# Kernel tuning notes

Hardware: AMD Instinct MI355X
Metric: run time of the kernel (lower is better)

## Reference

```python
import jax, jax.numpy as jnp
import numpy as np

WIDTHS = [2, 3, 5, 8, 13, 21, 34, 55, 89, 26]  # ragged one-hot feature widths, sum = 256
NSEG = len(WIDTHS)
B, IN = 8192, 256
LAYOUT = [1024, 1024, 1024, 256]
EPS = 1e-5  # BatchNorm1d default eps
TAU = 1.0


def setup_inputs() -> dict:
    key = jax.random.key(0)
    ks = iter(jax.random.split(key, 64))
    inp = {"x": jax.random.normal(next(ks), (B, IN), jnp.float32)}
    prev = IN
    for i, fc in enumerate(LAYOUT):
        inp[f"W{i}"] = jax.random.normal(next(ks), (fc, prev), jnp.float32) / np.float32(np.sqrt(prev))
        inp[f"b{i}"] = 0.01 * jax.random.normal(next(ks), (fc,), jnp.float32)
        if i + 1 < len(LAYOUT):  # Residual blocks carry BatchNorm params (eval mode)
            inp[f"g{i}"] = 1.0 + 0.1 * jax.random.normal(next(ks), (fc,), jnp.float32)
            inp[f"be{i}"] = 0.1 * jax.random.normal(next(ks), (fc,), jnp.float32)
            inp[f"rm{i}"] = 0.1 * jax.random.normal(next(ks), (fc,), jnp.float32)
            inp[f"rv{i}"] = 0.75 + 0.5 * jax.random.uniform(next(ks), (fc,), dtype=jnp.float32)
        prev += fc
    inp["seg_ids"] = jnp.asarray(np.repeat(np.arange(NSEG), WIDTHS), jnp.int32)  # [256]
    return inp


def _residual(x, W, b, g, be, rm, rv):
    # Linear -> eval-mode BatchNorm1d -> ReLU -> concat([out, input])
    h = x @ W.T + b
    h = (h - rm) * (g * jax.lax.rsqrt(rv + EPS)) + be
    return jnp.concatenate([jax.nn.relu(h), x], axis=1)


def _segment_softmax(x, seg_ids):
    # Fused segmented softmax over ragged feature groups (replaces per-feature Python loop)
    xt = x.T / TAU                                            # [F, B]
    m = jax.ops.segment_max(xt, seg_ids, num_segments=NSEG)   # [NSEG, B]
    e = jnp.exp(xt - m[seg_ids])
    s = jax.ops.segment_sum(e, seg_ids, num_segments=NSEG)
    return (e / s[seg_ids]).T                                 # [B, F]


def reference(x, W0, b0, g0, be0, rm0, rv0, W1, b1, g1, be1, rm1, rv1,
              W2, b2, g2, be2, rm2, rv2, W3, b3, seg_ids):
    h = _residual(x, W0, b0, g0, be0, rm0, rv0)   # [B, 1280]
    h = _residual(h, W1, b1, g1, be1, rm1, rv1)   # [B, 2304]
    h = _residual(h, W2, b2, g2, be2, rm2, rv2)   # [B, 3328]
    h = h @ W3.T + b3                              # [B, 256]
    return _segment_softmax(h, seg_ids)
```

## Files before the change

### kernel.cpp

```cpp
#include <hip/hip_runtime.h>
#include <hip/hip_fp16.h>


#define LDH 3328
#define NROWS 8192

typedef _Float16 f16x8 __attribute__((ext_vector_type(8)));
typedef _Float16 f16x4 __attribute__((ext_vector_type(4)));
typedef float f32x4 __attribute__((ext_vector_type(4)));

__constant__ int c_bnd[11] = {0, 2, 5, 10, 18, 31, 52, 86, 141, 230, 256};

__device__ __forceinline__ void async_cp16(const _Float16* g, _Float16* l) {
  __builtin_amdgcn_global_load_lds(
      (__attribute__((address_space(1))) void*)g,
      (__attribute__((address_space(3))) void*)l, 16, 0, 0);
}

__device__ __forceinline__ _Float16 f2h(float f) { return (_Float16)f; }

__global__ void prep_kernel(const float* __restrict__ s0,
                            const float* __restrict__ s1,
                            const float* __restrict__ s2,
                            const float* __restrict__ s3,
                            const float* __restrict__ x,
                            const float* __restrict__ b3,
                            _Float16* __restrict__ d0,
                            _Float16* __restrict__ d1,
                            _Float16* __restrict__ d2,
                            _Float16* __restrict__ d3,
                            _Float16* __restrict__ H, float* __restrict__ out,
                            int n0, int n1, int n2, int n3, int n4, int n5) {
  int i = blockIdx.x * blockDim.x + threadIdx.x;
  if (i >= n5) return;
  if (i >= n4) {
    const int j = i - n4;
    const int c = (j & 63) * 4;
    *(float4*)&out[(size_t)j * 4] = *(const float4*)&b3[c];
    return;
  }
  if (i >= n3) {
    const int j = i - n3;
    const int row = j >> 6;
    const int c = (j & 63) * 4;
    const float4 v = *(const float4*)&x[(size_t)j * 4];
    f16x4 h = {f2h(v.x), f2h(v.y), f2h(v.z), f2h(v.w)};
    *(f16x4*)&H[(size_t)row * LDH + 3072 + c] = h;
    return;
  }
  const float* s;
  _Float16* d;
  if (i < n0) {
    s = s0; d = d0;
  } else if (i < n1) {
    s = s1 - (size_t)n0 * 4; d = d1 - (size_t)n0 * 4;
  } else if (i < n2) {
    s = s2 - (size_t)n1 * 4; d = d2 - (size_t)n1 * 4;
  } else {
    s = s3 - (size_t)n2 * 4; d = d3 - (size_t)n2 * 4;
  }
  const float4 v = *(const float4*)&s[(size_t)i * 4];
  f16x4 h = {f2h(v.x), f2h(v.y), f2h(v.z), f2h(v.w)};
  *(f16x4*)&d[(size_t)i * 4] = h;
}

__launch_bounds__(256, 2) __global__
void gemm_bn_kernel(const _Float16* __restrict__ A, int K,
                    const _Float16* __restrict__ W,
                    const float* __restrict__ bias,
                    const float* __restrict__ g, const float* __restrict__ be,
                    const float* __restrict__ rm,
                    const float* __restrict__ rv, _Float16* __restrict__ outH,
                    int outOff) {
  __shared__ _Float16 Alds[128 * 128];
  __shared__ _Float16 Blds[128 * 128];

  const int tid = threadIdx.x;
  const int lane = tid & 63;
  const int wave = tid >> 6;
  const int wr = wave >> 1;
  const int wc = wave & 1;
  const int row0 = blockIdx.x * 128;
  const int col0 = blockIdx.y * 128;
  const int lr4 = lane >> 4;
  const int sl = lane & 15;
  const int fr = lane & 15;
  const int q = lane >> 4;

  f32x4 acc[4][4] = {};

  for (int k0 = 0; k0 < K; k0 += 128) {
    __syncthreads();
#pragma unroll
    for (int it = 0; it < 8; ++it) {
      const int j = it * 4 + wave;
      const int r = j * 4 + lr4;
      const int gc = sl ^ (r & 7);
      async_cp16(A + (size_t)(row0 + r) * LDH + k0 + gc * 8, &Alds[j * 512]);
      async_cp16(W + (size_t)(col0 + r) * K + k0 + gc * 8, &Blds[j * 512]);
    }
    __syncthreads();

#pragma unroll
    for (int kq = 0; kq < 4; ++kq) {
      f16x8 av[4], bv[4];
#pragma unroll
      for (int t = 0; t < 4; ++t) {
        const int ra = wr * 64 + t * 16 + fr;
        av[t] =
            *(const f16x8*)&Alds[ra * 128 + (((kq * 4 + q) ^ (ra & 7)) * 8)];
        const int rb = wc * 64 + t * 16 + fr;
        bv[t] =
            *(const f16x8*)&Blds[rb * 128 + (((kq * 4 + q) ^ (rb & 7)) * 8)];
      }
#pragma unroll
      for (int tm = 0; tm < 4; ++tm)
#pragma unroll
        for (int tn = 0; tn < 4; ++tn)
          acc[tm][tn] = __builtin_amdgcn_mfma_f32_16x16x32_f16(
              av[tm], bv[tn], acc[tm][tn], 0, 0, 0);
    }
  }

#pragma unroll
  for (int tn = 0; tn < 4; ++tn) {
    const int n = col0 + wc * 64 + tn * 16 + fr;
    const float alpha = g[n] * rsqrtf(rv[n] + 1e-5f);
    const float beta = (bias[n] - rm[n]) * alpha + be[n];
#pragma unroll
    for (int tm = 0; tm < 4; ++tm) {
      const int rbase = row0 + wr * 64 + tm * 16 + q * 4;
#pragma unroll
      for (int r = 0; r < 4; ++r) {
        float v = acc[tm][tn][r] * alpha + beta;
        v = fmaxf(v, 0.0f);
        outH[(size_t)(rbase + r) * LDH + outOff + n] = f2h(v);
      }
    }
  }
}

__launch_bounds__(256, 4) __global__
void gemm_out_kernel(const _Float16* __restrict__ A,
                     const _Float16* __restrict__ W,
                     float* __restrict__ out) {
  __shared__ _Float16 Alds[128 * 64];
  __shared__ _Float16 Blds[128 * 64];

  const int tid = threadIdx.x;
  const int lane = tid & 63;
  const int wave = tid >> 6;
  const int wr = wave >> 1;
  const int wc = wave & 1;
  const int row0 = blockIdx.x * 128;
  const int cb = blockIdx.y & 1;
  const int ks = blockIdx.y >> 1;
  const int col0 = cb * 128;
  const int k0b = ks * 832;
  const int k0e = k0b + 832;
  const int lr = lane >> 3;
  const int ls = lane & 7;
  const int lc = ls ^ lr;
  const int fr = lane & 15;
  const int q = lane >> 4;
  const int K = 3328;

  f32x4 acc[4][4] = {};

  for (int k0 = k0b; k0 < k0e; k0 += 64) {
    __syncthreads();
#pragma unroll
    for (int it = 0; it < 4; ++it) {
      const int rl = it * 32 + wave * 8;
      async_cp16(A + (size_t)(row0 + rl + lr) * LDH + k0 + lc * 8,
                 &Alds[rl * 64]);
      async_cp16(W + (size_t)(col0 + rl + lr) * K + k0 + lc * 8,
                 &Blds[rl * 64]);
    }
    __syncthreads();

#pragma unroll
    for (int kq = 0; kq < 2; ++kq) {
      f16x8 av[4], bv[4];
#pragma unroll
      for (int t = 0; t < 4; ++t) {
        const int ra = wr * 64 + t * 16 + fr;
        av[t] = *(const f16x8*)&Alds[ra * 64 + (((q + 4 * kq) ^ (ra & 7)) * 8)];
        const int rb = wc * 64 + t * 16 + fr;
        bv[t] = *(const f16x8*)&Blds[rb * 64 + (((q + 4 * kq) ^ (rb & 7)) * 8)];
      }
#pragma unroll
      for (int tm = 0; tm < 4; ++tm)
#pragma unroll
        for (int tn = 0; tn < 4; ++tn)
          acc[tm][tn] = __builtin_amdgcn_mfma_f32_16x16x32_f16(
              av[tm], bv[tn], acc[tm][tn], 0, 0, 0);
    }
  }

#pragma unroll
  for (int tn = 0; tn < 4; ++tn) {
    const int n = col0 + wc * 64 + tn * 16 + fr;
#pragma unroll
    for (int tm = 0; tm < 4; ++tm) {
      const int rbase = row0 + wr * 64 + tm * 16 + q * 4;
#pragma unroll
      for (int r = 0; r < 4; ++r)
        atomicAdd(&out[(size_t)(rbase + r) * 256 + n], acc[tm][tn][r]);
    }
  }
}

__global__ void segsoftmax_kernel(float* __restrict__ out,
                                  const int* __restrict__ segids) {
  __shared__ float vals[4][256];
  __shared__ float red[4][10];
  const int w = threadIdx.x >> 6;
  const int l = threadIdx.x & 63;
  const int row = blockIdx.x * 4 + w;
  float4 v = *(float4*)&out[(size_t)row * 256 + l * 4];
  *(float4*)&vals[w][l * 4] = v;
  __syncthreads();
  if (l < 10) {
    float m = -1e30f;
    for (int j = c_bnd[l]; j < c_bnd[l + 1]; ++j) m = fmaxf(m, vals[w][j]);
    red[w][l] = m;
  }
  __syncthreads();
  const int4 s4 = *(const int4*)&segids[l * 4];
  float4 e;
  e.x = expf(v.x - red[w][s4.x]);
  e.y = expf(v.y - red[w][s4.y]);
  e.z = expf(v.z - red[w][s4.z]);
  e.w = expf(v.w - red[w][s4.w]);
  *(float4*)&vals[w][l * 4] = e;
  __syncthreads();
  if (l < 10) {
    float s = 0.0f;
    for (int j = c_bnd[l]; j < c_bnd[l + 1]; ++j) s += vals[w][j];
    red[w][l] = s;
  }
  __syncthreads();
  float4 o;
  o.x = e.x / red[w][s4.x];
  o.y = e.y / red[w][s4.y];
  o.z = e.z / red[w][s4.z];
  o.w = e.w / red[w][s4.w];
  *(float4*)&out[(size_t)row * 256 + l * 4] = o;
}

extern "C" void kernel_launch(void* const* d_in, const int* in_sizes, int n_in,
                              void* d_out, int out_size, void* d_ws,
                              size_t ws_size, hipStream_t stream) {
  const float* x = (const float*)d_in[0];
  const float* W0 = (const float*)d_in[1];
  const float* b0 = (const float*)d_in[2];
  const float* g0 = (const float*)d_in[3];
  const float* be0 = (const float*)d_in[4];
  const float* rm0 = (const float*)d_in[5];
  const float* rv0 = (const float*)d_in[6];
  const float* W1 = (const float*)d_in[7];
  const float* b1 = (const float*)d_in[8];
  const float* g1 = (const float*)d_in[9];
  const float* be1 = (const float*)d_in[10];
  const float* rm1 = (const float*)d_in[11];
  const float* rv1 = (const float*)d_in[12];
  const float* W2 = (const float*)d_in[13];
  const float* b2 = (const float*)d_in[14];
  const float* g2 = (const float*)d_in[15];
  const float* be2 = (const float*)d_in[16];
  const float* rm2 = (const float*)d_in[17];
  const float* rv2 = (const float*)d_in[18];
  const float* W3 = (const float*)d_in[19];
  const float* b3 = (const float*)d_in[20];
  const int* seg = (const int*)d_in[21];
  float* out = (float*)d_out;

  _Float16* H = (_Float16*)d_ws;
  size_t off = (size_t)NROWS * LDH;
  _Float16* Wh0 = H + off; off += 1024 * 256;
  _Float16* Wh1 = H + off; off += 1024 * 1280;
  _Float16* Wh2 = H + off; off += 1024 * 2304;
  _Float16* Wh3 = H + off;

  const int n0 = 65536, n1 = n0 + 327680, n2 = n1 + 589824, n3 = n2 + 212992;
  const int n4 = n3 + 524288, n5 = n4 + 524288;
  prep_kernel<<<(n5 + 255) / 256, 256, 0, stream>>>(
      W0, W1, W2, W3, x, b3, Wh0, Wh1, Wh2, Wh3, H, out, n0, n1, n2, n3, n4,
      n5);

  dim3 blk(256);
  gemm_bn_kernel<<<dim3(64, 8), blk, 0, stream>>>(
      H + 3072, 256, Wh0, b0, g0, be0, rm0, rv0, H, 2048);
  gemm_bn_kernel<<<dim3(64, 8), blk, 0, stream>>>(
      H + 2048, 1280, Wh1, b1, g1, be1, rm1, rv1, H, 1024);
  gemm_bn_kernel<<<dim3(64, 8), blk, 0, stream>>>(
      H + 1024, 2304, Wh2, b2, g2, be2, rm2, rv2, H, 0);
  gemm_out_kernel<<<dim3(64, 8), blk, 0, stream>>>(H, Wh3, out);
  segsoftmax_kernel<<<2048, 256, 0, stream>>>(out, seg);
}
```

Before: 243.4 us.

## Rewrite GEMMs as triple-buffered 8-wave pipelined kernels with 256x128 tiles

Replaces the synchronous load-then-compute GEMM loops with a shared gemm_loop that triple-buffers 64-wide K slices in dynamic LDS. Next-slice global-to-LDS copies are interleaved with four MFMA sub-phases, using explicit vmcnt waits, barriers and setprio. Blocks grow to 512 threads covering 256 rows, which halves the grid and lets the B tile be shared across more rows. This aims to hide memory latency behind MFMA work, at the cost of 144KB LDS per block, heavy barrier use and fewer blocks in flight.

After: 256.6 us. +5.4%, slower.

```diff
diff --git a/kernel.cpp b/kernel.cpp
--- a/kernel.cpp
+++ b/kernel.cpp
@@ -64,63 +64,139 @@
   *(f16x4*)&d[(size_t)i * 4] = h;
 }
 
-__launch_bounds__(256, 2) __global__
-void gemm_bn_kernel(const _Float16* __restrict__ A, int K,
-                    const _Float16* __restrict__ W,
-                    const float* __restrict__ bias,
-                    const float* __restrict__ g, const float* __restrict__ be,
-                    const float* __restrict__ rm,
-                    const float* __restrict__ rv, _Float16* __restrict__ outH,
-                    int outOff) {
-  __shared__ _Float16 Alds[128 * 128];
-  __shared__ _Float16 Blds[128 * 128];
-
+
+#define BUFSZ 24576
+#define ABOFF 16384
+
+#define STA(Ab, q, k0)                                                       \
+  async_cp16(A + (size_t)(row0 + (q) * 64 + srow) * LDH + (k0) + sgc,        \
+             (Ab) + ((q) * 64 + wave * 8) * 64)
+#define STB(Bb, h, k0)                                                       \
+  async_cp16(W + (size_t)(col0 + (h) * 64 + srow) * K + (k0) + sgc,          \
+             (Bb) + ((h) * 64 + wave * 8) * 64)
+
+#define LOADQ(QM, QN)                                                        \
+  {                                                                          \
+    const int ra0 = wr * 64 + (QM) * 32 + fr;                                \
+    const int ra1 = ra0 + 16;                                                \
+    const int rb0 = wc * 64 + (QN) * 32 + fr;                                \
+    const int rb1 = rb0 + 16;                                                \
+    av[0][0] = *(const f16x8*)&Ac[ra0 * 64 + ((q2 ^ (ra0 & 7)) * 8)];        \
+    av[0][1] = *(const f16x8*)&Ac[ra0 * 64 + (((q2 + 4) ^ (ra0 & 7)) * 8)];  \
+    av[1][0] = *(const f16x8*)&Ac[ra1 * 64 + ((q2 ^ (ra1 & 7)) * 8)];        \
+    av[1][1] = *(const f16x8*)&Ac[ra1 * 64 + (((q2 + 4) ^ (ra1 & 7)) * 8)];  \
+    bv[0][0] = *(const f16x8*)&Bc[rb0 * 64 + ((q2 ^ (rb0 & 7)) * 8)];        \
+    bv[0][1] = *(const f16x8*)&Bc[rb0 * 64 + (((q2 + 4) ^ (rb0 & 7)) * 8)];  \
+    bv[1][0] = *(const f16x8*)&Bc[rb1 * 64 + ((q2 ^ (rb1 & 7)) * 8)];        \
+    bv[1][1] = *(const f16x8*)&Bc[rb1 * 64 + (((q2 + 4) ^ (rb1 & 7)) * 8)];  \
+  }
+
+#define MF(a, b, c) __builtin_amdgcn_mfma_f32_16x16x32_f16(a, b, c, 0, 0, 0)
+
+#define MFMAQ(QM, QN)                                                         \
+  __builtin_amdgcn_s_setprio(1);                                              \
+  acc[(QM)*2+0][(QN)*2+0] = MF(av[0][0], bv[0][0], acc[(QM)*2+0][(QN)*2+0]);  \
+  acc[(QM)*2+0][(QN)*2+1] = MF(av[0][0], bv[1][0], acc[(QM)*2+0][(QN)*2+1]);  \
+  acc[(QM)*2+1][(QN)*2+0] = MF(av[1][0], bv[0][0], acc[(QM)*2+1][(QN)*2+0]);  \
+  acc[(QM)*2+1][(QN)*2+1] = MF(av[1][0], bv[1][0], acc[(QM)*2+1][(QN)*2+1]);  \
+  acc[(QM)*2+0][(QN)*2+0] = MF(av[0][1], bv[0][1], acc[(QM)*2+0][(QN)*2+0]);  \
+  acc[(QM)*2+0][(QN)*2+1] = MF(av[0][1], bv[1][1], acc[(QM)*2+0][(QN)*2+1]);  \
+  acc[(QM)*2+1][(QN)*2+0] = MF(av[1][1], bv[0][1], acc[(QM)*2+1][(QN)*2+0]);  \
+  acc[(QM)*2+1][(QN)*2+1] = MF(av[1][1], bv[1][1], acc[(QM)*2+1][(QN)*2+1]);  \
+  __builtin_amdgcn_s_setprio(0);
+
+#define GITER(VMSTR, ISS, k0n)                                               \
+  {                                                                          \
+    _Float16* Ac = lds_ + cur * BUFSZ;                                       \
+    _Float16* Bc = Ac + ABOFF;                                               \
+    _Float16* An = lds_ + nxt * BUFSZ;                                       \
+    _Float16* Bn = An + ABOFF;                                               \
+    f16x8 av[2][2], bv[2][2];                                                \
+    if (ISS) { STA(An, 0, k0n); STA(An, 1, k0n); }                           \
+    asm volatile("s_waitcnt " VMSTR ::: "memory");                           \
+    __builtin_amdgcn_s_barrier();                                            \
+    LOADQ(0, 0);                                                             \
+    MFMAQ(0, 0);                                                             \
+    __builtin_amdgcn_s_barrier();                                            \
+    if (ISS) { STA(An, 2, k0n); STA(An, 3, k0n); }                           \
+    LOADQ(0, 1);                                                             \
+    __builtin_amdgcn_s_barrier();                                            \
+    MFMAQ(0, 1);                                                             \
+    __builtin_amdgcn_s_barrier();                                            \
+    if (ISS) { STB(Bn, 0, k0n); }                                            \
+    LOADQ(1, 0);                                                             \
+    __builtin_amdgcn_s_barrier();                                            \
+    MFMAQ(1, 0);                                                             \
+    __builtin_amdgcn_s_barrier();                                            \
+    if (ISS) { STB(Bn, 1, k0n); }                                            \
+    LOADQ(1, 1);                                                             \
+    __builtin_amdgcn_s_barrier();                                            \
+    MFMAQ(1, 1);                                                             \
+    __builtin_amdgcn_s_barrier();                                            \
+  }
+
+__device__ __forceinline__ void gemm_loop(const _Float16* __restrict__ A,
+                                          const _Float16* __restrict__ W,
+                                          int K, int kbase, int nt, int row0,
+                                          int col0, int tid, _Float16* lds_,
+                                          f32x4 (&acc)[4][4]) {
+  const int lane = tid & 63;
+  const int wave = tid >> 6;
+  const int wr = wave >> 1;
+  const int wc = wave & 1;
+  const int fr = lane & 15;
+  const int q2 = lane >> 4;
+  const int srow = tid >> 3;
+  const int sgc = ((tid & 7) ^ (srow & 7)) * 8;
+
+  {
+    _Float16* A0 = lds_;
+    _Float16* B0 = lds_ + ABOFF;
+    STA(A0, 0, kbase); STA(A0, 1, kbase); STA(A0, 2, kbase); STA(A0, 3, kbase);
+    STB(B0, 0, kbase); STB(B0, 1, kbase);
+    _Float16* A1 = lds_ + BUFSZ;
+    _Float16* B1 = A1 + ABOFF;
+    STA(A1, 0, kbase + 64); STA(A1, 1, kbase + 64);
+    STA(A1, 2, kbase + 64); STA(A1, 3, kbase + 64);
+    STB(B1, 0, kbase + 64); STB(B1, 1, kbase + 64);
+  }
+
+  int cur = 0, nxt = 2;
+  int t = 0;
+  for (; t + 2 < nt; ++t) {
+    const int k0n = kbase + (t + 2) * 64;
+    GITER("vmcnt(8)", 1, k0n);
+    cur = cur == 2 ? 0 : cur + 1;
+    nxt = nxt == 2 ? 0 : nxt + 1;
+  }
+  {
+    const int k0n = 0;
+    GITER("vmcnt(6)", 0, k0n);
+    cur = cur == 2 ? 0 : cur + 1;
+    GITER("vmcnt(0)", 0, k0n);
+  }
+}
+
+__launch_bounds__(512, 2) __global__
+void gemm_bn_8ph(const _Float16* __restrict__ A, int K,
+                 const _Float16* __restrict__ W,
+                 const float* __restrict__ bias,
+                 const float* __restrict__ g, const float* __restrict__ be,
+                 const float* __restrict__ rm, const float* __restrict__ rv,
+                 _Float16* __restrict__ outH, int outOff) {
+  extern __shared__ _Float16 lds_[];
   const int tid = threadIdx.x;
   const int lane = tid & 63;
   const int wave = tid >> 6;
   const int wr = wave >> 1;
   const int wc = wave & 1;
-  const int row0 = blockIdx.x * 128;
+  const int fr = lane & 15;
+  const int q2 = lane >> 4;
+  const int row0 = blockIdx.x * 256;
   const int col0 = blockIdx.y * 128;
-  const int lr4 = lane >> 4;
-  const int sl = lane & 15;
-  const int fr = lane & 15;
-  const int q = lane >> 4;
 
   f32x4 acc[4][4] = {};
-
-  for (int k0 = 0; k0 < K; k0 += 128) {
-    __syncthreads();
-#pragma unroll
-    for (int it = 0; it < 8; ++it) {
-      const int j = it * 4 + wave;
-      const int r = j * 4 + lr4;
-      const int gc = sl ^ (r & 7);
-      async_cp16(A + (size_t)(row0 + r) * LDH + k0 + gc * 8, &Alds[j * 512]);
-      async_cp16(W + (size_t)(col0 + r) * K + k0 + gc * 8, &Blds[j * 512]);
-    }
-    __syncthreads();
-
-#pragma unroll
-    for (int kq = 0; kq < 4; ++kq) {
-      f16x8 av[4], bv[4];
-#pragma unroll
-      for (int t = 0; t < 4; ++t) {
-        const int ra = wr * 64 + t * 16 + fr;
-        av[t] =
-            *(const f16x8*)&Alds[ra * 128 + (((kq * 4 + q) ^ (ra & 7)) * 8)];
-        const int rb = wc * 64 + t * 16 + fr;
-        bv[t] =
-            *(const f16x8*)&Blds[rb * 128 + (((kq * 4 + q) ^ (rb & 7)) * 8)];
-      }
-#pragma unroll
-      for (int tm = 0; tm < 4; ++tm)
-#pragma unroll
-        for (int tn = 0; tn < 4; ++tn)
-          acc[tm][tn] = __builtin_amdgcn_mfma_f32_16x16x32_f16(
-              av[tm], bv[tn], acc[tm][tn], 0, 0, 0);
-    }
-  }
+  gemm_loop(A, W, K, 0, K >> 6, row0, col0, tid, lds_, acc);
 
 #pragma unroll
   for (int tn = 0; tn < 4; ++tn) {
@@ -129,7 +205,7 @@
     const float beta = (bias[n] - rm[n]) * alpha + be[n];
 #pragma unroll
     for (int tm = 0; tm < 4; ++tm) {
-      const int rbase = row0 + wr * 64 + tm * 16 + q * 4;
+      const int rbase = row0 + wr * 64 + tm * 16 + q2 * 4;
 #pragma unroll
       for (int r = 0; r < 4; ++r) {
         float v = acc[tm][tn][r] * alpha + beta;
@@ -140,70 +216,32 @@
   }
 }
 
-__launch_bounds__(256, 4) __global__
-void gemm_out_kernel(const _Float16* __restrict__ A,
-                     const _Float16* __restrict__ W,
-                     float* __restrict__ out) {
-  __shared__ _Float16 Alds[128 * 64];
-  __shared__ _Float16 Blds[128 * 64];
-
+__launch_bounds__(512, 2) __global__
+void gemm_out_8ph(const _Float16* __restrict__ A,
+                  const _Float16* __restrict__ W, float* __restrict__ out) {
+  extern __shared__ _Float16 lds_[];
   const int tid = threadIdx.x;
   const int lane = tid & 63;
   const int wave = tid >> 6;
   const int wr = wave >> 1;
   const int wc = wave & 1;
-  const int row0 = blockIdx.x * 128;
+  const int fr = lane & 15;
+  const int q2 = lane >> 4;
+  const int row0 = blockIdx.x * 256;
   const int cb = blockIdx.y & 1;
   const int ks = blockIdx.y >> 1;
   const int col0 = cb * 128;
-  const int k0b = ks * 832;
-  const int k0e = k0b + 832;
-  const int lr = lane >> 3;
-  const int ls = lane & 7;
-  const int lc = ls ^ lr;
-  const int fr = lane & 15;
-  const int q = lane >> 4;
   const int K = 3328;
 
   f32x4 acc[4][4] = {};
-
-  for (int k0 = k0b; k0 < k0e; k0 += 64) {
-    __syncthreads();
-#pragma unroll
-    for (int it = 0; it < 4; ++it) {
-      const int rl = it * 32 + wave * 8;
-      async_cp16(A + (size_t)(row0 + rl + lr) * LDH + k0 + lc * 8,
-                 &Alds[rl * 64]);
-      async_cp16(W + (size_t)(col0 + rl + lr) * K + k0 + lc * 8,
-                 &Blds[rl * 64]);
-    }
-    __syncthreads();
-
-#pragma unroll
-    for (int kq = 0; kq < 2; ++kq) {
-      f16x8 av[4], bv[4];
-#pragma unroll
-      for (int t = 0; t < 4; ++t) {
-        const int ra = wr * 64 + t * 16 + fr;
-        av[t] = *(const f16x8*)&Alds[ra * 64 + (((q + 4 * kq) ^ (ra & 7)) * 8)];
-        const int rb = wc * 64 + t * 16 + fr;
-        bv[t] = *(const f16x8*)&Blds[rb * 64 + (((q + 4 * kq) ^ (rb & 7)) * 8)];
-      }
-#pragma unroll
-      for (int tm = 0; tm < 4; ++tm)
-#pragma unroll
-        for (int tn = 0; tn < 4; ++tn)
-          acc[tm][tn] = __builtin_amdgcn_mfma_f32_16x16x32_f16(
-              av[tm], bv[tn], acc[tm][tn], 0, 0, 0);
-    }
-  }
+  gemm_loop(A, W, K, ks * 832, 13, row0, col0, tid, lds_, acc);
 
 #pragma unroll
   for (int tn = 0; tn < 4; ++tn) {
     const int n = col0 + wc * 64 + tn * 16 + fr;
 #pragma unroll
     for (int tm = 0; tm < 4; ++tm) {
-      const int rbase = row0 + wr * 64 + tm * 16 + q * 4;
+      const int rbase = row0 + wr * 64 + tm * 16 + q2 * 4;
 #pragma unroll
       for (int r = 0; r < 4; ++r)
         atomicAdd(&out[(size_t)(rbase + r) * 256 + n], acc[tm][tn][r]);
@@ -283,19 +321,27 @@
   _Float16* Wh2 = H + off; off += 1024 * 2304;
   _Float16* Wh3 = H + off;
 
+  static bool attr_done = false;
+  if (!attr_done) {
+    hipFuncSetAttribute(reinterpret_cast<const void*>(gemm_bn_8ph),
+                        hipFuncAttributeMaxDynamicSharedMemorySize, 147456);
+    hipFuncSetAttribute(reinterpret_cast<const void*>(gemm_out_8ph),
+                        hipFuncAttributeMaxDynamicSharedMemorySize, 147456);
+    attr_done = true;
+  }
+
   const int n0 = 65536, n1 = n0 + 327680, n2 = n1 + 589824, n3 = n2 + 212992;
   const int n4 = n3 + 524288, n5 = n4 + 524288;
   prep_kernel<<<(n5 + 255) / 256, 256, 0, stream>>>(
       W0, W1, W2, W3, x, b3, Wh0, Wh1, Wh2, Wh3, H, out, n0, n1, n2, n3, n4,
       n5);
 
-  dim3 blk(256);
-  gemm_bn_kernel<<<dim3(64, 8), blk, 0, stream>>>(
+  gemm_bn_8ph<<<dim3(32, 8), 512, 147456, stream>>>(
       H + 3072, 256, Wh0, b0, g0, be0, rm0, rv0, H, 2048);
-  gemm_bn_kernel<<<dim3(64, 8), blk, 0, stream>>>(
+  gemm_bn_8ph<<<dim3(32, 8), 512, 147456, stream>>>(
       H + 2048, 1280, Wh1, b1, g1, be1, rm1, rv1, H, 1024);
-  gemm_bn_kernel<<<dim3(64, 8), blk, 0, stream>>>(
+  gemm_bn_8ph<<<dim3(32, 8), 512, 147456, stream>>>(
       H + 1024, 2304, Wh2, b2, g2, be2, rm2, rv2, H, 0);
-  gemm_out_kernel<<<dim3(64, 8), blk, 0, stream>>>(H, Wh3, out);
+  gemm_out_8ph<<<dim3(32, 8), 512, 147456, stream>>>(H, Wh3, out);
   segsoftmax_kernel<<<2048, 256, 0, stream>>>(out, seg);
 }
```
